# Performance work log

Hardware: AMD Instinct MI355X
Metric: run time of the kernel (lower is better)

Reference implementation:

```python
import jax, jax.numpy as jnp
import numpy as np

N_NODES = 100000

def _sage_layer(x, src, dst, W_self, W_neigh, b, act):
    # DGL SAGEConv 'mean': h = fc_self(x) + fc_neigh(mean_{u->v} x_u) + bias
    msg_sum = jax.ops.segment_sum(x[src], dst, num_segments=N_NODES)  # [N, d]
    deg = jax.ops.segment_sum(jnp.ones((src.shape[0], 1), x.dtype), dst, num_segments=N_NODES)
    h_neigh = msg_sum / jnp.maximum(deg, 1.0)
    h = x @ W_self + h_neigh @ W_neigh + b
    return jax.nn.relu(h) if act else h

def _edge_score(h, s, d, W1, b1, W2, b2):
    e = jnp.concatenate([h[s], h[d]], axis=-1)  # [E, 2*64]
    return (jax.nn.relu(e @ W1 + b1) @ W2 + b2).squeeze(-1)  # [E]

def setup_inputs() -> dict:
    key = jax.random.key(0)
    ks = jax.random.split(key, 16)
    E, EP = 1000000, 200000
    d_in, d_hid, d_out = 512, 256, 64
    def lin(k, fan_in, shape):
        return jax.random.normal(k, shape, dtype=jnp.float32) * (1.0 / np.sqrt(fan_in))
    return {
        "x": jax.random.normal(ks[0], (N_NODES, d_in), dtype=jnp.float32),
        "src": jax.random.randint(ks[1], (E,), 0, N_NODES, dtype=jnp.int32),
        "dst": jax.random.randint(ks[2], (E,), 0, N_NODES, dtype=jnp.int32),
        "pos_src": jax.random.randint(ks[3], (EP,), 0, N_NODES, dtype=jnp.int32),
        "pos_dst": jax.random.randint(ks[4], (EP,), 0, N_NODES, dtype=jnp.int32),
        "neg_src": jax.random.randint(ks[5], (EP,), 0, N_NODES, dtype=jnp.int32),
        "neg_dst": jax.random.randint(ks[6], (EP,), 0, N_NODES, dtype=jnp.int32),
        "W_self1": lin(ks[7], d_in, (d_in, d_hid)),
        "W_neigh1": lin(ks[8], d_in, (d_in, d_hid)),
        "b1": jnp.zeros((d_hid,), jnp.float32),
        "W_self2": lin(ks[9], d_hid, (d_hid, d_out)),
        "W_neigh2": lin(ks[10], d_hid, (d_hid, d_out)),
        "b2": jnp.zeros((d_out,), jnp.float32),
        "Wp1": lin(ks[11], 2 * d_out, (2 * d_out, d_out)),
        "bp1": jnp.zeros((d_out,), jnp.float32),
        "Wp2": lin(ks[12], d_out, (d_out, 1)),
        "bp2": jnp.zeros((1,), jnp.float32),
    }

def reference(x, src, dst, pos_src, pos_dst, neg_src, neg_dst,
              W_self1, W_neigh1, b1, W_self2, W_neigh2, b2,
              Wp1, bp1, Wp2, bp2):
    h = _sage_layer(x, src, dst, W_self1, W_neigh1, b1, act=True)
    h = _sage_layer(h, src, dst, W_self2, W_neigh2, b2, act=False)
    pos_score = _edge_score(h, pos_src, pos_dst, Wp1, bp1, Wp2, bp2)
    neg_score = _edge_score(h, neg_src, neg_dst, Wp1, bp1, Wp2, bp2)
    return (pos_score, neg_score)
```

## Files before the change

kernel.cpp:

```cpp
#include <hip/hip_runtime.h>
#include <hip/hip_bf16.h>


#define N_NODES 100000
#define N_EDGES 1000000
#define EPOS    200000
#define NSB     391

typedef unsigned short u16;
typedef unsigned int   u32;

typedef __bf16 bf16x8 __attribute__((ext_vector_type(8)));
typedef float  f32x4  __attribute__((ext_vector_type(4)));
typedef u16    u16x8  __attribute__((ext_vector_type(8)));

__device__ __forceinline__ u16 f2bf(float f) {
  u32 u = __float_as_uint(f);
  u32 r = (u + 0x7fffu + ((u >> 16) & 1u)) >> 16;
  return (u16)r;
}
__device__ __forceinline__ float bf2f(u16 h) {
  return __uint_as_float(((u32)h) << 16);
}

__global__ __launch_bounds__(256) void k_x2bf(const float* __restrict__ in,
                                              u16* __restrict__ out) {
  long i = ((long)blockIdx.x * 256 + threadIdx.x) * 8;
  float4 f0 = *(const float4*)(in + i);
  float4 f1 = *(const float4*)(in + i + 4);
  u16x8 o;
  o[0] = f2bf(f0.x); o[1] = f2bf(f0.y); o[2] = f2bf(f0.z); o[3] = f2bf(f0.w);
  o[4] = f2bf(f1.x); o[5] = f2bf(f1.y); o[6] = f2bf(f1.z); o[7] = f2bf(f1.w);
  *(u16x8*)(out + i) = o;
}

__global__ void k_w1t(const float* __restrict__ Ws, const float* __restrict__ Wn,
                      u16* __restrict__ W1t) {
  int idx = blockIdx.x * 256 + threadIdx.x;
  int j = idx >> 9, k = idx & 511;
  float v = (j < 256) ? Ws[k * 256 + j] : Wn[k * 256 + (j - 256)];
  W1t[idx] = f2bf(v);
}
__global__ void k_w2t(const float* __restrict__ Ws, const float* __restrict__ Wn,
                      u16* __restrict__ W2t) {
  int idx = blockIdx.x * 256 + threadIdx.x;
  int j = idx >> 8, k = idx & 255;
  float v = (j < 64) ? Ws[k * 64 + j] : Wn[k * 64 + (j - 64)];
  W2t[idx] = f2bf(v);
}
__global__ void k_wpt(const float* __restrict__ Wp1, u16* __restrict__ Wpt) {
  int idx = blockIdx.x * 256 + threadIdx.x;
  int j = idx >> 6, k = idx & 63;
  float v = (j < 64) ? Wp1[k * 64 + j] : Wp1[(64 + k) * 64 + (j - 64)];
  Wpt[idx] = f2bf(v);
}

__global__ void k_deg(const int* __restrict__ dst, int* __restrict__ deg,
                      int* __restrict__ epos) {
  int i = blockIdx.x * 256 + threadIdx.x;
  if (i < N_EDGES) epos[i] = atomicAdd(&deg[dst[i]], 1);
}

__global__ __launch_bounds__(256) void k_scan_a(const int* __restrict__ deg,
                                                int* __restrict__ bsum) {
  __shared__ int s[256];
  int i = blockIdx.x * 256 + threadIdx.x;
  s[threadIdx.x] = (i < N_NODES) ? deg[i] : 0;
  __syncthreads();
  for (int off = 128; off > 0; off >>= 1) {
    if (threadIdx.x < off) s[threadIdx.x] += s[threadIdx.x + off];
    __syncthreads();
  }
  if (threadIdx.x == 0) bsum[blockIdx.x] = s[0];
}

__global__ __launch_bounds__(512) void k_scan_b(int* __restrict__ bsum) {
  __shared__ int s[512];
  const int t = threadIdx.x;
  int v = (t < NSB) ? bsum[t] : 0;
  s[t] = v;
  __syncthreads();
  for (int off = 1; off < 512; off <<= 1) {
    int w = (t >= off) ? s[t - off] : 0;
    __syncthreads();
    s[t] += w;
    __syncthreads();
  }
  if (t < NSB) bsum[t] = s[t] - v;
}

__global__ __launch_bounds__(256) void k_scan_c(const int* __restrict__ deg,
                                                const int* __restrict__ bsum,
                                                int* __restrict__ offs,
                                                float* __restrict__ invdeg) {
  __shared__ int s[256];
  const int t = threadIdx.x;
  const int i = blockIdx.x * 256 + t;
  const int d = (i < N_NODES) ? deg[i] : 0;
  s[t] = d;
  __syncthreads();
  for (int off = 1; off < 256; off <<= 1) {
    int w = (t >= off) ? s[t - off] : 0;
    __syncthreads();
    s[t] += w;
    __syncthreads();
  }
  if (i < N_NODES) {
    const int base = bsum[blockIdx.x];
    offs[i] = base + s[t] - d;
    invdeg[i] = 1.0f / (float)(d > 0 ? d : 1);
    if (i == N_NODES - 1) offs[N_NODES] = base + s[t];
  }
}

__global__ void k_fill(const int* __restrict__ src, const int* __restrict__ dst,
                       const int* __restrict__ offs, const int* __restrict__ epos,
                       int* __restrict__ csr) {
  int i = blockIdx.x * 256 + threadIdx.x;
  if (i < N_EDGES) csr[offs[dst[i]] + epos[i]] = src[i];
}

template <bool OUT_F32>
__global__ __launch_bounds__(256) void gemm_bt(const u16* __restrict__ A,
                                               const u16* __restrict__ Bt,
                                               void* __restrict__ Cv,
                                               int M, int N, int K) {
  __shared__ u16 As[128 * 32];
  __shared__ u16 Bs[128 * 32];
  const int tid  = threadIdx.x;
  const int lane = tid & 63;
  const int wid  = tid >> 6;
  const int wr   = wid >> 1, wc = wid & 1;
  const int bm0  = blockIdx.y * 128;
  const int bn0  = blockIdx.x * 128;

  const int sr = tid >> 2;
  const int sc = (tid & 3) * 8;
  const long ar0 = (long)min(bm0 + sr,      M - 1) * K + sc;
  const long ar1 = (long)min(bm0 + sr + 64, M - 1) * K + sc;
  const long br0 = (long)(bn0 + sr)      * K + sc;
  const long br1 = (long)(bn0 + sr + 64) * K + sc;

  f32x4 acc[4][4];
#pragma unroll
  for (int i = 0; i < 4; ++i)
#pragma unroll
    for (int j = 0; j < 4; ++j) {
      f32x4 z = {0.f, 0.f, 0.f, 0.f};
      acc[i][j] = z;
    }

  uint4 a0 = *(const uint4*)(A + ar0);
  uint4 a1 = *(const uint4*)(A + ar1);
  uint4 b0 = *(const uint4*)(Bt + br0);
  uint4 b1 = *(const uint4*)(Bt + br1);

  const int nk = K >> 5;
  for (int kk = 0; kk < nk; ++kk) {
    *(uint4*)&As[sr * 32 + sc]        = a0;
    *(uint4*)&As[(sr + 64) * 32 + sc] = a1;
    *(uint4*)&Bs[sr * 32 + sc]        = b0;
    *(uint4*)&Bs[(sr + 64) * 32 + sc] = b1;
    __syncthreads();
    if (kk + 1 < nk) {
      const int k0 = (kk + 1) << 5;
      a0 = *(const uint4*)(A + ar0 + k0);
      a1 = *(const uint4*)(A + ar1 + k0);
      b0 = *(const uint4*)(Bt + br0 + k0);
      b1 = *(const uint4*)(Bt + br1 + k0);
    }
    bf16x8 af[4], bfr[4];
#pragma unroll
    for (int mi = 0; mi < 4; ++mi)
      af[mi] = *reinterpret_cast<const bf16x8*>(
          &As[(wr * 64 + mi * 16 + (lane & 15)) * 32 + ((lane >> 4) * 8)]);
#pragma unroll
    for (int ni = 0; ni < 4; ++ni)
      bfr[ni] = *reinterpret_cast<const bf16x8*>(
          &Bs[(wc * 64 + ni * 16 + (lane & 15)) * 32 + ((lane >> 4) * 8)]);
#pragma unroll
    for (int mi = 0; mi < 4; ++mi)
#pragma unroll
      for (int ni = 0; ni < 4; ++ni)
        acc[mi][ni] = __builtin_amdgcn_mfma_f32_16x16x32_bf16(
            af[mi], bfr[ni], acc[mi][ni], 0, 0, 0);
    __syncthreads();
  }

  const int colb = bn0 + wc * 64 + (lane & 15);
  const int rowb = bm0 + wr * 64 + ((lane >> 4) * 4);
#pragma unroll
  for (int mi = 0; mi < 4; ++mi) {
#pragma unroll
    for (int ni = 0; ni < 4; ++ni) {
      const int col = colb + ni * 16;
#pragma unroll
      for (int e = 0; e < 4; ++e) {
        const int row = rowb + mi * 16 + e;
        if (row < M) {
          if (OUT_F32)
            ((float*)Cv)[(long)row * N + col] = acc[mi][ni][e];
          else
            ((u16*)Cv)[(long)row * N + col] = f2bf(acc[mi][ni][e]);
        }
      }
    }
  }
}

__global__ __launch_bounds__(256) void k_agg1(const u16* __restrict__ z1b,
                                              const int* __restrict__ csr,
                                              const int* __restrict__ offs,
                                              const float* __restrict__ invdeg,
                                              const float* __restrict__ b1,
                                              u16* __restrict__ h1b) {
  const int v = blockIdx.x;
  const int c = threadIdx.x;
  const int o0 = offs[v], o1 = offs[v + 1];
  float acc = 0.f;
  int i = o0;
  for (; i + 4 <= o1; i += 4) {
    const int u0 = csr[i], u1 = csr[i + 1], u2 = csr[i + 2], u3 = csr[i + 3];
    float p0 = bf2f(z1b[(long)u0 * 512 + 256 + c]);
    float p1 = bf2f(z1b[(long)u1 * 512 + 256 + c]);
    float p2 = bf2f(z1b[(long)u2 * 512 + 256 + c]);
    float p3 = bf2f(z1b[(long)u3 * 512 + 256 + c]);
    acc += (p0 + p1) + (p2 + p3);
  }
  for (; i < o1; ++i)
    acc += bf2f(z1b[(long)csr[i] * 512 + 256 + c]);
  float h = bf2f(z1b[(long)v * 512 + c]) + acc * invdeg[v] + b1[c];
  h1b[(long)v * 256 + c] = f2bf(fmaxf(h, 0.f));
}

__global__ __launch_bounds__(256) void k_agg2(const u16* __restrict__ z2b,
                                              const int* __restrict__ csr,
                                              const int* __restrict__ offs,
                                              const float* __restrict__ invdeg,
                                              const float* __restrict__ b2,
                                              u16* __restrict__ h2b) {
  const int v = blockIdx.x * 4 + (threadIdx.x >> 6);
  const int c = threadIdx.x & 63;
  const int o0 = offs[v], o1 = offs[v + 1];
  float acc = 0.f;
  int i = o0;
  for (; i + 4 <= o1; i += 4) {
    const int u0 = csr[i], u1 = csr[i + 1], u2 = csr[i + 2], u3 = csr[i + 3];
    float p0 = bf2f(z2b[(long)u0 * 128 + 64 + c]);
    float p1 = bf2f(z2b[(long)u1 * 128 + 64 + c]);
    float p2 = bf2f(z2b[(long)u2 * 128 + 64 + c]);
    float p3 = bf2f(z2b[(long)u3 * 128 + 64 + c]);
    acc += (p0 + p1) + (p2 + p3);
  }
  for (; i < o1; ++i)
    acc += bf2f(z2b[(long)csr[i] * 128 + 64 + c]);
  float h = bf2f(z2b[(long)v * 128 + c]) + acc * invdeg[v] + b2[c];
  h2b[(long)v * 64 + c] = f2bf(h);
}

__global__ __launch_bounds__(256) void k_edge(const float* __restrict__ UV,
                                              const int* __restrict__ ps,
                                              const int* __restrict__ pd,
                                              const int* __restrict__ ns,
                                              const int* __restrict__ nd,
                                              const float* __restrict__ bp1,
                                              const float* __restrict__ Wp2,
                                              const float* __restrict__ bp2,
                                              float* __restrict__ out) {
  const int g = blockIdx.x * 4 + (threadIdx.x >> 6);
  const int j = threadIdx.x & 63;
  int s, d;
  if (g < EPOS) { s = ps[g]; d = pd[g]; }
  else          { s = ns[g - EPOS]; d = nd[g - EPOS]; }
  float t = UV[(long)s * 128 + j] + UV[(long)d * 128 + 64 + j] + bp1[j];
  float r = fmaxf(t, 0.f) * Wp2[j];
#pragma unroll
  for (int off = 32; off > 0; off >>= 1) r += __shfl_down(r, off, 64);
  if (j == 0) out[g] = r + bp2[0];
}

extern "C" void kernel_launch(void* const* d_in, const int* in_sizes, int n_in,
                              void* d_out, int out_size, void* d_ws, size_t ws_size,
                              hipStream_t stream) {
  const float* x   = (const float*)d_in[0];
  const int*   src = (const int*)d_in[1];
  const int*   dst = (const int*)d_in[2];
  const int*   ps  = (const int*)d_in[3];
  const int*   pd  = (const int*)d_in[4];
  const int*   ns  = (const int*)d_in[5];
  const int*   nd  = (const int*)d_in[6];
  const float* Ws1 = (const float*)d_in[7];
  const float* Wn1 = (const float*)d_in[8];
  const float* b1  = (const float*)d_in[9];
  const float* Ws2 = (const float*)d_in[10];
  const float* Wn2 = (const float*)d_in[11];
  const float* b2  = (const float*)d_in[12];
  const float* Wp1 = (const float*)d_in[13];
  const float* bp1 = (const float*)d_in[14];
  const float* Wp2 = (const float*)d_in[15];
  const float* bp2 = (const float*)d_in[16];
  float* out = (float*)d_out;

  char* ws = (char*)d_ws;
  const size_t RB = 102400000;
  const size_t RC = 204800000;
  u16*   xb  = (u16*)(ws);
  u16*   h1b = (u16*)(ws);
  float* UV  = (float*)(ws + 51200000);
  int*   epos= (int*)(ws + RB);
  u16*   z1b = (u16*)(ws + RB);
  u16*   z2b = (u16*)(ws + RB);
  u16*   h2b = (u16*)(ws + RB + 25600000);
  size_t o = RC;
  u16*   W1t = (u16*)(ws + o); o += 524288;
  u16*   W2t = (u16*)(ws + o); o += 65536;
  u16*   Wpt = (u16*)(ws + o); o += 16384;
  int*   deg = (int*)(ws + o); o += 400128;
  int*   offs= (int*)(ws + o); o += 400128;
  float* idg = (float*)(ws + o); o += 400128;
  int*   bsum= (int*)(ws + o); o += 2048;
  int*   csr = (int*)(ws + o); o += 4000000;
  (void)ws_size; (void)in_sizes; (void)n_in; (void)out_size;

  hipMemsetAsync(deg, 0, 400128, stream);

  k_x2bf<<<25000, 256, 0, stream>>>(x, xb);
  k_w1t<<<1024, 256, 0, stream>>>(Ws1, Wn1, W1t);
  k_w2t<<<128, 256, 0, stream>>>(Ws2, Wn2, W2t);
  k_wpt<<<32, 256, 0, stream>>>(Wp1, Wpt);
  k_deg<<<3907, 256, 0, stream>>>(dst, deg, epos);
  k_scan_a<<<NSB, 256, 0, stream>>>(deg, bsum);
  k_scan_b<<<1, 512, 0, stream>>>(bsum);
  k_scan_c<<<NSB, 256, 0, stream>>>(deg, bsum, offs, idg);
  k_fill<<<3907, 256, 0, stream>>>(src, dst, offs, epos, csr);

  gemm_bt<false><<<dim3(4, 782), 256, 0, stream>>>(xb, W1t, z1b, N_NODES, 512, 512);
  k_agg1<<<100000, 256, 0, stream>>>(z1b, csr, offs, idg, b1, h1b);
  gemm_bt<false><<<dim3(1, 782), 256, 0, stream>>>(h1b, W2t, z2b, N_NODES, 128, 256);
  k_agg2<<<25000, 256, 0, stream>>>(z2b, csr, offs, idg, b2, h2b);
  gemm_bt<true><<<dim3(1, 782), 256, 0, stream>>>(h2b, Wpt, UV, N_NODES, 128, 64);
  k_edge<<<100000, 256, 0, stream>>>(UV, ps, pd, ns, nd, bp1, Wp2, bp2, out);
}
```

Before: 774.5 us.

## Double-buffer GEMM via direct LDS loads, vectorize aggregation and edge kernels

The GEMM now stages A/B tiles with global_load_lds into double-buffered shared memory, so the next k-tile loads while the current one computes and staging registers go away. Aggregation layer 1 handles four nodes per block with 4-wide bf16 loads per lane, and layer 2 splits each node's neighbors across two half-waves with 2-wide loads. The UV projection is stored in bf16 instead of fp32, and the edge scorer reads packed pairs through half-wave shuffles, halving the bytes it gathers. In exchange the edge path loses some precision, and the LDS staging layout relies on the wave-ordered addressing of global_load_lds matching the old row layout.

```diff
diff --git a/kernel.cpp b/kernel.cpp
--- a/kernel.cpp
+++ b/kernel.cpp
@@ -21,6 +21,12 @@
 }
 __device__ __forceinline__ float bf2f(u16 h) {
   return __uint_as_float(((u32)h) << 16);
+}
+
+__device__ __forceinline__ void gl_lds16(const void* g, void* l) {
+  __builtin_amdgcn_global_load_lds(
+      (const __attribute__((address_space(1))) void*)g,
+      (__attribute__((address_space(3))) void*)l, 16, 0, 0);
 }
 
 __global__ __launch_bounds__(256) void k_x2bf(const float* __restrict__ in,
@@ -125,8 +131,8 @@
                                                const u16* __restrict__ Bt,
                                                void* __restrict__ Cv,
                                                int M, int N, int K) {
-  __shared__ u16 As[128 * 32];
-  __shared__ u16 Bs[128 * 32];
+  __shared__ u16 As[2][4096];
+  __shared__ u16 Bs[2][4096];
   const int tid  = threadIdx.x;
   const int lane = tid & 63;
   const int wid  = tid >> 6;
@@ -136,10 +142,11 @@
 
   const int sr = tid >> 2;
   const int sc = (tid & 3) * 8;
-  const long ar0 = (long)min(bm0 + sr,      M - 1) * K + sc;
-  const long ar1 = (long)min(bm0 + sr + 64, M - 1) * K + sc;
-  const long br0 = (long)(bn0 + sr)      * K + sc;
-  const long br1 = (long)(bn0 + sr + 64) * K + sc;
+  const u16* pa0 = A  + (long)min(bm0 + sr,      M - 1) * K + sc;
+  const u16* pa1 = A  + (long)min(bm0 + sr + 64, M - 1) * K + sc;
+  const u16* pb0 = Bt + (long)(bn0 + sr)      * K + sc;
+  const u16* pb1 = Bt + (long)(bn0 + sr + 64) * K + sc;
+  const int lw = wid * 512;
 
   f32x4 acc[4][4];
 #pragma unroll
@@ -150,34 +157,27 @@
       acc[i][j] = z;
     }
 
-  uint4 a0 = *(const uint4*)(A + ar0);
-  uint4 a1 = *(const uint4*)(A + ar1);
-  uint4 b0 = *(const uint4*)(Bt + br0);
-  uint4 b1 = *(const uint4*)(Bt + br1);
-
   const int nk = K >> 5;
+#define STAGE(buf, kk) do { const int k0_ = (kk) << 5;                    \
+    gl_lds16(pa0 + k0_, &As[buf][lw]);                                    \
+    gl_lds16(pa1 + k0_, &As[buf][2048 + lw]);                             \
+    gl_lds16(pb0 + k0_, &Bs[buf][lw]);                                    \
+    gl_lds16(pb1 + k0_, &Bs[buf][2048 + lw]); } while (0)
+
+  STAGE(0, 0);
+  __syncthreads();
+  int cur = 0;
   for (int kk = 0; kk < nk; ++kk) {
-    *(uint4*)&As[sr * 32 + sc]        = a0;
-    *(uint4*)&As[(sr + 64) * 32 + sc] = a1;
-    *(uint4*)&Bs[sr * 32 + sc]        = b0;
-    *(uint4*)&Bs[(sr + 64) * 32 + sc] = b1;
-    __syncthreads();
-    if (kk + 1 < nk) {
-      const int k0 = (kk + 1) << 5;
-      a0 = *(const uint4*)(A + ar0 + k0);
-      a1 = *(const uint4*)(A + ar1 + k0);
-      b0 = *(const uint4*)(Bt + br0 + k0);
-      b1 = *(const uint4*)(Bt + br1 + k0);
-    }
+    if (kk + 1 < nk) STAGE(cur ^ 1, kk + 1);
     bf16x8 af[4], bfr[4];
 #pragma unroll
     for (int mi = 0; mi < 4; ++mi)
       af[mi] = *reinterpret_cast<const bf16x8*>(
-          &As[(wr * 64 + mi * 16 + (lane & 15)) * 32 + ((lane >> 4) * 8)]);
+          &As[cur][(wr * 64 + mi * 16 + (lane & 15)) * 32 + ((lane >> 4) * 8)]);
 #pragma unroll
     for (int ni = 0; ni < 4; ++ni)
       bfr[ni] = *reinterpret_cast<const bf16x8*>(
-          &Bs[(wc * 64 + ni * 16 + (lane & 15)) * 32 + ((lane >> 4) * 8)]);
+          &Bs[cur][(wc * 64 + ni * 16 + (lane & 15)) * 32 + ((lane >> 4) * 8)]);
 #pragma unroll
     for (int mi = 0; mi < 4; ++mi)
 #pragma unroll
@@ -185,7 +185,9 @@
         acc[mi][ni] = __builtin_amdgcn_mfma_f32_16x16x32_bf16(
             af[mi], bfr[ni], acc[mi][ni], 0, 0, 0);
     __syncthreads();
-  }
+    cur ^= 1;
+  }
+#undef STAGE
 
   const int colb = bn0 + wc * 64 + (lane & 15);
   const int rowb = bm0 + wr * 64 + ((lane >> 4) * 4);
@@ -214,23 +216,36 @@
                                               const float* __restrict__ invdeg,
                                               const float* __restrict__ b1,
                                               u16* __restrict__ h1b) {
-  const int v = blockIdx.x;
-  const int c = threadIdx.x;
+  const int v    = blockIdx.x * 4 + (threadIdx.x >> 6);
+  const int lane = threadIdx.x & 63;
+  const int c    = lane * 4;
   const int o0 = offs[v], o1 = offs[v + 1];
-  float acc = 0.f;
+  float a0 = 0.f, a1 = 0.f, a2 = 0.f, a3 = 0.f;
   int i = o0;
   for (; i + 4 <= o1; i += 4) {
     const int u0 = csr[i], u1 = csr[i + 1], u2 = csr[i + 2], u3 = csr[i + 3];
-    float p0 = bf2f(z1b[(long)u0 * 512 + 256 + c]);
-    float p1 = bf2f(z1b[(long)u1 * 512 + 256 + c]);
-    float p2 = bf2f(z1b[(long)u2 * 512 + 256 + c]);
-    float p3 = bf2f(z1b[(long)u3 * 512 + 256 + c]);
-    acc += (p0 + p1) + (p2 + p3);
-  }
-  for (; i < o1; ++i)
-    acc += bf2f(z1b[(long)csr[i] * 512 + 256 + c]);
-  float h = bf2f(z1b[(long)v * 512 + c]) + acc * invdeg[v] + b1[c];
-  h1b[(long)v * 256 + c] = f2bf(fmaxf(h, 0.f));
+    ushort4 q0 = *(const ushort4*)&z1b[(long)u0 * 512 + 256 + c];
+    ushort4 q1 = *(const ushort4*)&z1b[(long)u1 * 512 + 256 + c];
+    ushort4 q2 = *(const ushort4*)&z1b[(long)u2 * 512 + 256 + c];
+    ushort4 q3 = *(const ushort4*)&z1b[(long)u3 * 512 + 256 + c];
+    a0 += (bf2f(q0.x) + bf2f(q1.x)) + (bf2f(q2.x) + bf2f(q3.x));
+    a1 += (bf2f(q0.y) + bf2f(q1.y)) + (bf2f(q2.y) + bf2f(q3.y));
+    a2 += (bf2f(q0.z) + bf2f(q1.z)) + (bf2f(q2.z) + bf2f(q3.z));
+    a3 += (bf2f(q0.w) + bf2f(q1.w)) + (bf2f(q2.w) + bf2f(q3.w));
+  }
+  for (; i < o1; ++i) {
+    ushort4 q = *(const ushort4*)&z1b[(long)csr[i] * 512 + 256 + c];
+    a0 += bf2f(q.x); a1 += bf2f(q.y); a2 += bf2f(q.z); a3 += bf2f(q.w);
+  }
+  const float w = invdeg[v];
+  ushort4 sf = *(const ushort4*)&z1b[(long)v * 512 + c];
+  float4 bb = *(const float4*)&b1[c];
+  ushort4 o;
+  o.x = f2bf(fmaxf(bf2f(sf.x) + a0 * w + bb.x, 0.f));
+  o.y = f2bf(fmaxf(bf2f(sf.y) + a1 * w + bb.y, 0.f));
+  o.z = f2bf(fmaxf(bf2f(sf.z) + a2 * w + bb.z, 0.f));
+  o.w = f2bf(fmaxf(bf2f(sf.w) + a3 * w + bb.w, 0.f));
+  *(ushort4*)&h1b[(long)v * 256 + c] = o;
 }
 
 __global__ __launch_bounds__(256) void k_agg2(const u16* __restrict__ z2b,
@@ -239,26 +254,30 @@
                                               const float* __restrict__ invdeg,
                                               const float* __restrict__ b2,
                                               u16* __restrict__ h2b) {
-  const int v = blockIdx.x * 4 + (threadIdx.x >> 6);
-  const int c = threadIdx.x & 63;
+  const int v    = blockIdx.x * 4 + (threadIdx.x >> 6);
+  const int lane = threadIdx.x & 63;
+  const int half = lane >> 5;
+  const int c    = (lane & 31) * 2;
   const int o0 = offs[v], o1 = offs[v + 1];
-  float acc = 0.f;
-  int i = o0;
-  for (; i + 4 <= o1; i += 4) {
-    const int u0 = csr[i], u1 = csr[i + 1], u2 = csr[i + 2], u3 = csr[i + 3];
-    float p0 = bf2f(z2b[(long)u0 * 128 + 64 + c]);
-    float p1 = bf2f(z2b[(long)u1 * 128 + 64 + c]);
-    float p2 = bf2f(z2b[(long)u2 * 128 + 64 + c]);
-    float p3 = bf2f(z2b[(long)u3 * 128 + 64 + c]);
-    acc += (p0 + p1) + (p2 + p3);
-  }
-  for (; i < o1; ++i)
-    acc += bf2f(z2b[(long)csr[i] * 128 + 64 + c]);
-  float h = bf2f(z2b[(long)v * 128 + c]) + acc * invdeg[v] + b2[c];
-  h2b[(long)v * 64 + c] = f2bf(h);
-}
-
-__global__ __launch_bounds__(256) void k_edge(const float* __restrict__ UV,
+  float a0 = 0.f, a1 = 0.f;
+  for (int i = o0 + half; i < o1; i += 2) {
+    const u32 q = *(const u32*)&z2b[(long)csr[i] * 128 + 64 + c];
+    a0 += bf2f((u16)q);
+    a1 += bf2f((u16)(q >> 16));
+  }
+  a0 += __shfl_xor(a0, 32);
+  a1 += __shfl_xor(a1, 32);
+  if (half == 0) {
+    const float w = invdeg[v];
+    const u32 sq = *(const u32*)&z2b[(long)v * 128 + c];
+    float h0 = bf2f((u16)sq) + a0 * w + b2[c];
+    float h1 = bf2f((u16)(sq >> 16)) + a1 * w + b2[c + 1];
+    u32 o = (u32)f2bf(h0) | ((u32)f2bf(h1) << 16);
+    *(u32*)&h2b[(long)v * 64 + c] = o;
+  }
+}
+
+__global__ __launch_bounds__(256) void k_edge(const u16* __restrict__ UVb,
                                               const int* __restrict__ ps,
                                               const int* __restrict__ pd,
                                               const int* __restrict__ ns,
@@ -267,16 +286,24 @@
                                               const float* __restrict__ Wp2,
                                               const float* __restrict__ bp2,
                                               float* __restrict__ out) {
-  const int g = blockIdx.x * 4 + (threadIdx.x >> 6);
-  const int j = threadIdx.x & 63;
+  const int g    = blockIdx.x * 4 + (threadIdx.x >> 6);
+  const int lane = threadIdx.x & 63;
+  const int half = lane >> 5;
+  const int l    = lane & 31;
   int s, d;
   if (g < EPOS) { s = ps[g]; d = pd[g]; }
   else          { s = ns[g - EPOS]; d = nd[g - EPOS]; }
-  float t = UV[(long)s * 128 + j] + UV[(long)d * 128 + 64 + j] + bp1[j];
-  float r = fmaxf(t, 0.f) * Wp2[j];
-#pragma unroll
-  for (int off = 32; off > 0; off >>= 1) r += __shfl_down(r, off, 64);
-  if (j == 0) out[g] = r + bp2[0];
+  const int node = half ? d : s;
+  const u32 q = *(const u32*)&UVb[(long)node * 128 + half * 64 + 2 * l];
+  float t0 = bf2f((u16)q), t1 = bf2f((u16)(q >> 16));
+  t0 += __shfl_xor(t0, 32);
+  t1 += __shfl_xor(t1, 32);
+  const float2 bb = *(const float2*)&bp1[2 * l];
+  const float2 ww = *(const float2*)&Wp2[2 * l];
+  float p = fmaxf(t0 + bb.x, 0.f) * ww.x + fmaxf(t1 + bb.y, 0.f) * ww.y;
+#pragma unroll
+  for (int off = 16; off > 0; off >>= 1) p += __shfl_xor(p, off);
+  if (lane == 0) out[g] = p + bp2[0];
 }
 
 extern "C" void kernel_launch(void* const* d_in, const int* in_sizes, int n_in,
@@ -306,7 +333,7 @@
   const size_t RC = 204800000;
   u16*   xb  = (u16*)(ws);
   u16*   h1b = (u16*)(ws);
-  float* UV  = (float*)(ws + 51200000);
+  u16*   UVb = (u16*)(ws + 51200000);
   int*   epos= (int*)(ws + RB);
   u16*   z1b = (u16*)(ws + RB);
   u16*   z2b = (u16*)(ws + RB);
@@ -335,9 +362,9 @@
   k_fill<<<3907, 256, 0, stream>>>(src, dst, offs, epos, csr);
 
   gemm_bt<false><<<dim3(4, 782), 256, 0, stream>>>(xb, W1t, z1b, N_NODES, 512, 512);
-  k_agg1<<<100000, 256, 0, stream>>>(z1b, csr, offs, idg, b1, h1b);
+  k_agg1<<<25000, 256, 0, stream>>>(z1b, csr, offs, idg, b1, h1b);
   gemm_bt<false><<<dim3(1, 782), 256, 0, stream>>>(h1b, W2t, z2b, N_NODES, 128, 256);
   k_agg2<<<25000, 256, 0, stream>>>(z2b, csr, offs, idg, b2, h2b);
-  gemm_bt<true><<<dim3(1, 782), 256, 0, stream>>>(h2b, Wpt, UV, N_NODES, 128, 64);
-  k_edge<<<100000, 256, 0, stream>>>(UV, ps, pd, ns, nd, bp1, Wp2, bp2, out);
-}
+  gemm_bt<false><<<dim3(1, 782), 256, 0, stream>>>(h2b, Wpt, UVb, N_NODES, 128, 64);
+  k_edge<<<100000, 256, 0, stream>>>(UVb, ps, pd, ns, nd, bp1, Wp2, bp2, out);
+}
```

Result: faster. 740.2 us (-4.4%).
